# Kernel optimization log

Hardware: AMD Instinct MI355X
Metric: run time of the kernel (lower is better)

The kernel has to match this reference:

```python
import jax, jax.numpy as jnp
import numpy as np

B, N, IN_DIM, H, D = 4, 2048, 128, 4, 64
LEAKY_SLOPE = 0.2
BN_EPS = 1e-5


def setup_inputs() -> dict:
    key = jax.random.key(0)
    k_h, k_W, k_a, k_adj = jax.random.split(key, 4)
    h = jax.random.normal(k_h, (B, N, IN_DIM), dtype=jnp.float32)
    # Linear weight (no bias): stored as [in_dim, H*D] for x @ W
    W = jax.random.normal(k_W, (IN_DIM, H * D), dtype=jnp.float32) * (1.0 / np.sqrt(IN_DIM))
    # attention vector a: [H, 2D] (xavier-ish scale)
    a = jax.random.normal(k_a, (H, 2 * D), dtype=jnp.float32) * (1.0 / np.sqrt(2 * D))
    # BatchNorm affine params (training-mode batch stats used in reference)
    gamma = jnp.ones((H * D,), dtype=jnp.float32)
    beta = jnp.zeros((H * D,), dtype=jnp.float32)
    adj = jax.random.randint(k_adj, (N, N), 0, 2, dtype=jnp.int32)
    return {"h": h, "W": W, "a": a, "gamma": gamma, "beta": beta, "adj": adj}


def reference(h, W, a, gamma, beta, adj):
    Bs, Ns, _ = h.shape
    # Wh: [B, H, N, D]
    Wh = (h @ W).reshape(Bs, Ns, H, D).transpose(0, 2, 1, 3)
    # Algebraic decomposition of the concat-attention:
    # e[b,h,i,j] = leaky(Wh[b,h,i]. a[h,:D] + Wh[b,h,j]. a[h,D:])
    src = jnp.einsum("bhnd,hd->bhn", Wh, a[:, :D])  # query-node term
    dst = jnp.einsum("bhnd,hd->bhn", Wh, a[:, D:])  # key-node term
    e = src[:, :, :, None] + dst[:, :, None, :]      # [B,H,N,N]
    e = jnp.where(e >= 0, e, LEAKY_SLOPE * e)        # LeakyReLU
    mask = (adj == 0)[None, None, :, :]
    e = jnp.where(mask, -jnp.inf, e)
    alpha = jax.nn.softmax(e, axis=-1)
    alpha = jnp.nan_to_num(alpha, nan=0.0)
    # dropout is identity in eval mode (deterministic reference)
    h_new = jnp.einsum("bhij,bhjd->bhid", alpha, Wh)  # [B,H,N,D]
    h_new = h_new.transpose(0, 2, 1, 3).reshape(Bs, Ns, H * D)
    # BatchNorm1d (training mode: biased batch statistics over B*N rows)
    flat = h_new.reshape(Bs * Ns, H * D)
    mean = jnp.mean(flat, axis=0)
    var = jnp.mean(jnp.square(flat - mean), axis=0)
    flat = (flat - mean) * jax.lax.rsqrt(var + BN_EPS) * gamma + beta
    out = flat.reshape(Bs, Ns, H * D)
    return jax.nn.elu(out)
```

## Files before the change

### kernel.cpp

```cpp
#include <hip/hip_runtime.h>

#define B_ 4
#define N_ 2048
#define IND_ 128
#define H_ 4
#define D_ 64
#define HD_ 256
#define LEAKY 0.2f
#define BNEPS 1e-5f
#define LOG2E 1.44269504088896340736f

typedef float f32x4 __attribute__((ext_vector_type(4)));
typedef short s16x8 __attribute__((ext_vector_type(8)));
typedef unsigned int u32x4 __attribute__((ext_vector_type(4)));

static __device__ __forceinline__ unsigned short f2bf(float f) {
  unsigned u = __builtin_bit_cast(unsigned, f);
  u = (u + 0x7fffu + ((u >> 16) & 1u)) >> 16;
  return (unsigned short)u;
}

__global__ __launch_bounds__(256) void k_pack_adj(const int* __restrict__ adj,
                                                  unsigned* __restrict__ bits,
                                                  float* __restrict__ zbuf,
                                                  const float* __restrict__ W,
                                                  unsigned short* __restrict__ wt) {
  if (blockIdx.x == 0) {
    for (int i = threadIdx.x; i < 512; i += 256) zbuf[i] = 0.f;
  }
  if (blockIdx.x < 128) {
    int kb = blockIdx.x;
    wt[(size_t)threadIdx.x * 128 + kb] = f2bf(W[(size_t)kb * 256 + threadIdx.x]);
  }
  int idx = blockIdx.x * 256 + threadIdx.x;
  int val = adj[idx] != 0;
  unsigned long long m = __ballot(val);
  int lane = threadIdx.x & 63;
  if (lane == 0)       bits[idx >> 5] = (unsigned)m;
  else if (lane == 32) bits[idx >> 5] = (unsigned)(m >> 32);
}

__global__ __launch_bounds__(256) void k_gemm(const float* __restrict__ h,
                                              const unsigned short* __restrict__ wt,
                                              const float* __restrict__ a,
                                              unsigned short* __restrict__ wht,
                                              float* __restrict__ src,
                                              float* __restrict__ dst) {
  int t = threadIdx.x;
  int w = t >> 6, lane = t & 63, m = lane & 15, g = lane >> 4;
  int r0 = blockIdx.x * 16;
  int b = r0 >> 11, n0 = r0 & 2047;
  int hh = w;

  s16x8 Af[4][4];
  const s16x8* wtp = (const s16x8*)wt;
#pragma unroll
  for (int chf = 0; chf < 4; chf++) {
    int ch = w * 64 + chf * 16 + m;
#pragma unroll
    for (int ks = 0; ks < 4; ks++)
      Af[chf][ks] = wtp[(ch * 128 + ks * 32 + g * 8) >> 3];
  }
  s16x8 Bf[4];
#pragma unroll
  for (int ks = 0; ks < 4; ks++) {
    const float* hp = h + (size_t)(r0 + m) * 128 + ks * 32 + g * 8;
    f32x4 h0 = *(const f32x4*)hp;
    f32x4 h1 = *(const f32x4*)(hp + 4);
    u32x4 bu;
#pragma unroll
    for (int e = 0; e < 4; e++) {
      float lo = (e < 2) ? h0[2 * e] : h1[2 * e - 4];
      float hi = (e < 2) ? h0[2 * e + 1] : h1[2 * e - 3];
      unsigned rr_;
      asm("v_cvt_pk_bf16_f32 %0, %1, %2" : "=v"(rr_) : "v"(lo), "v"(hi));
      bu[e] = rr_;
    }
    Bf[ks] = __builtin_bit_cast(s16x8, bu);
  }

  f32x4 acc[4];
#pragma unroll
  for (int chf = 0; chf < 4; chf++) acc[chf] = (f32x4){0.f, 0.f, 0.f, 0.f};
#pragma unroll
  for (int ks = 0; ks < 4; ks++)
#pragma unroll
    for (int chf = 0; chf < 4; chf++)
      acc[chf] = __builtin_amdgcn_mfma_f32_16x16x32_bf16(Af[chf][ks], Bf[ks], acc[chf], 0, 0, 0);

  size_t obase = ((size_t)((b * 4 + hh) * 64)) * 2048 + n0 + m;
#pragma unroll
  for (int chf = 0; chf < 4; chf++) {
    int d = chf * 16 + g * 4;
#pragma unroll
    for (int reg = 0; reg < 4; reg++)
      wht[obase + (size_t)(d + reg) * 2048] = f2bf(acc[chf][reg]);
  }

  float sv = 0.f, dv = 0.f;
#pragma unroll
  for (int chf = 0; chf < 4; chf++)
#pragma unroll
    for (int reg = 0; reg < 4; reg++) {
      int d = chf * 16 + g * 4 + reg;
      float whv = acc[chf][reg];
      sv = fmaf(whv, a[hh * 128 + d] * LOG2E, sv);
      dv = fmaf(whv, a[hh * 128 + 64 + d] * LOG2E, dv);
    }
  sv += __shfl_xor(sv, 16); sv += __shfl_xor(sv, 32);
  dv += __shfl_xor(dv, 16); dv += __shfl_xor(dv, 32);
  if (g == 0) {
    src[(size_t)(b * 4 + hh) * 2048 + n0 + m] = sv;
    dst[(size_t)(b * 4 + hh) * 2048 + n0 + m] = dv;
  }
}

__global__ __launch_bounds__(256) void k_attn(const unsigned* __restrict__ adjb,
                                              const unsigned short* __restrict__ wht,
                                              const float* __restrict__ src,
                                              const float* __restrict__ dst,
                                              float* __restrict__ hnew,
                                              float* __restrict__ chsum,
                                              float* __restrict__ chsq) {
  __shared__ unsigned adj_lds[64 * 65];
  __shared__ u32x4 whb4[1024];
  __shared__ float ul[2048], vl[2048];
  __shared__ float redS[256], redQ[256];

  int t = threadIdx.x;
  int bid = blockIdx.x;
  int bh = bid & 15, it = bid >> 4;
  int b = bh >> 2, hh = bh & 3;
  int i0 = it * 64;
  int w = t >> 6, lane = t & 63, m = lane & 15, g = lane >> 4;

  for (int idx = t; idx < 64 * 64; idx += 256) {
    int r = idx >> 6, wd = idx & 63;
    adj_lds[r * 65 + wd] = adjb[(size_t)(i0 + r) * 64 + wd];
  }
  {
    const f32x4* dg = (const f32x4*)(dst + (size_t)bh * 2048);
    f32x4 d0 = dg[2 * t], d1 = dg[2 * t + 1];
    f32x4 u0, u1, v0, v1;
#pragma unroll
    for (int e = 0; e < 4; e++) {
      u0[e] = __builtin_amdgcn_exp2f(d0[e]);
      v0[e] = __builtin_amdgcn_exp2f(0.2f * d0[e]);
      u1[e] = __builtin_amdgcn_exp2f(d1[e]);
      v1[e] = __builtin_amdgcn_exp2f(0.2f * d1[e]);
    }
    ((f32x4*)ul)[2 * t] = u0;  ((f32x4*)ul)[2 * t + 1] = u1;
    ((f32x4*)vl)[2 * t] = v0;  ((f32x4*)vl)[2 * t + 1] = v1;
  }

  float srcL = src[(size_t)bh * 2048 + i0 + w * 16 + m];
  float Af = __builtin_amdgcn_exp2f(srcL);
  float Bf = __builtin_amdgcn_exp2f(LEAKY * srcL);

  s16x8 bones;
#pragma unroll
  for (int e = 0; e < 8; e++) bones[e] = (short)0x3F80;

  f32x4 acc[4], accd;
#pragma unroll
  for (int db = 0; db < 4; db++) acc[db] = (f32x4){0.f, 0.f, 0.f, 0.f};
  accd = (f32x4){0.f, 0.f, 0.f, 0.f};

  char* wbase = (char*)whb4;
  int r_ = t >> 2, ch_ = t & 3;
  const char* gbase = (const char*)(wht + (size_t)(bh * 64 + r_) * 2048);
  int sw = (r_ & 7) << 4;
  u32x4 R0, R1;

#define LOADT(jt_) { const u32x4* gp = (const u32x4*)(gbase + (size_t)(jt_) * 128 + ch_ * 32); \
                     R0 = gp[0]; R1 = gp[1]; }
#define WRITET(pb_) { char* wb_ = (pb_); \
                      *(u32x4*)(wb_ + r_ * 128 + ((ch_ * 32) ^ sw)) = R0; \
                      *(u32x4*)(wb_ + r_ * 128 + ((ch_ * 32 + 16) ^ sw)) = R1; }

  LOADT(0); WRITET(wbase); LOADT(1);

  for (int jt = 0; jt < 32; jt++) {
    int cur = jt & 1;
    __syncthreads();
    if (jt < 31) WRITET(wbase + (cur ^ 1) * 8192);
    if (jt < 30) LOADT(jt + 2);
    const char* wbufc = wbase + cur * 8192;

#pragma unroll
    for (int ks = 0; ks < 2; ks++) {
      unsigned adjw = adj_lds[(w * 16 + m) * 65 + jt * 2 + ks];
      unsigned bits = (adjw >> (g * 8)) & 0xffu;
      const float* up = &ul[jt * 64 + ks * 32 + g * 8];
      const float* vp = &vl[jt * 64 + ks * 32 + g * 8];
      f32x4 u0 = *(const f32x4*)up, u1 = *(const f32x4*)(up + 4);
      f32x4 v0 = *(const f32x4*)vp, v1 = *(const f32x4*)(vp + 4);
      float pm[8];
#pragma unroll
      for (int e = 0; e < 8; e++) {
        float ue = (e < 4) ? u0[e] : u1[e - 4];
        float ve = (e < 4) ? v0[e] : v1[e - 4];
        float p = fmaxf(Af * ue, Bf * ve);
        unsigned keep = (unsigned)(((int)(bits << (31 - e))) >> 31);
        pm[e] = __builtin_bit_cast(float, __builtin_bit_cast(unsigned, p) & keep);
      }
      u32x4 afu;
#pragma unroll
      for (int e2 = 0; e2 < 4; e2++) {
        unsigned rr_;
        asm("v_cvt_pk_bf16_f32 %0, %1, %2" : "=v"(rr_) : "v"(pm[2 * e2]), "v"(pm[2 * e2 + 1]));
        afu[e2] = rr_;
      }
      s16x8 af = __builtin_bit_cast(s16x8, afu);
#pragma unroll
      for (int db = 0; db < 4; db++) {
        int dl = db * 16 + m;
        int off = dl * 128 + ((ks * 64 + g * 16) ^ ((dl & 7) << 4));
        s16x8 bf = *(const s16x8*)(wbufc + off);
        acc[db] = __builtin_amdgcn_mfma_f32_16x16x32_bf16(af, bf, acc[db], 0, 0, 0);
      }
      accd = __builtin_amdgcn_mfma_f32_16x16x32_bf16(af, bones, accd, 0, 0, 0);
    }
  }
#undef LOADT
#undef WRITET

  float sums[4] = {0.f, 0.f, 0.f, 0.f}, sqs[4] = {0.f, 0.f, 0.f, 0.f};
#pragma unroll
  for (int r = 0; r < 4; r++) {
    float inv = accd[r] > 0.f ? 1.0f / accd[r] : 0.f;
    int n = i0 + w * 16 + 4 * g + r;
#pragma unroll
    for (int db = 0; db < 4; db++) {
      float val = acc[db][r] * inv;
      hnew[(size_t)(b * 2048 + n) * 256 + hh * 64 + db * 16 + m] = val;
      sums[db] += val;
      sqs[db] += val * val;
    }
  }
#pragma unroll
  for (int db = 0; db < 4; db++) {
    sums[db] += __shfl_xor(sums[db], 16); sums[db] += __shfl_xor(sums[db], 32);
    sqs[db]  += __shfl_xor(sqs[db], 16);  sqs[db]  += __shfl_xor(sqs[db], 32);
  }
  if (g == 0) {
#pragma unroll
    for (int db = 0; db < 4; db++) {
      redS[w * 64 + db * 16 + m] = sums[db];
      redQ[w * 64 + db * 16 + m] = sqs[db];
    }
  }
  __syncthreads();
  if (t < 64) {
    float ts2 = redS[t] + redS[64 + t] + redS[128 + t] + redS[192 + t];
    float tq = redQ[t] + redQ[64 + t] + redQ[128 + t] + redQ[192 + t];
    atomicAdd(&chsum[hh * 64 + t], ts2);
    atomicAdd(&chsq[hh * 64 + t], tq);
  }
}

__global__ __launch_bounds__(256) void k_bn_elu(const float* __restrict__ hnew,
                                                const float* __restrict__ chsum,
                                                const float* __restrict__ chsq,
                                                const float* __restrict__ gamma,
                                                const float* __restrict__ beta,
                                                float* __restrict__ out) {
  int idx4 = blockIdx.x * 256 + threadIdx.x;
  f32x4 x = ((const f32x4*)hnew)[idx4];
  int c0 = (idx4 * 4) & 255;
  f32x4 s = *(const f32x4*)(chsum + c0);
  f32x4 sq = *(const f32x4*)(chsq + c0);
  f32x4 gm = *(const f32x4*)(gamma + c0);
  f32x4 bt = *(const f32x4*)(beta + c0);
  f32x4 y;
#pragma unroll
  for (int e = 0; e < 4; e++) {
    float mean = s[e] * (1.0f / 8192.0f);
    float var = sq[e] * (1.0f / 8192.0f) - mean * mean;
    float sc = gm[e] * rsqrtf(var + BNEPS);
    float v = (x[e] - mean) * sc + bt[e];
    y[e] = v > 0.f ? v : expm1f(v);
  }
  ((f32x4*)out)[idx4] = y;
}

extern "C" void kernel_launch(void* const* d_in, const int* in_sizes, int n_in,
                              void* d_out, int out_size, void* d_ws, size_t ws_size,
                              hipStream_t stream) {
  const float* h = (const float*)d_in[0];
  const float* W = (const float*)d_in[1];
  const float* a = (const float*)d_in[2];
  const float* gamma = (const float*)d_in[3];
  const float* beta = (const float*)d_in[4];
  const int* adj = (const int*)d_in[5];

  char* ws = (char*)d_ws;
  unsigned* adjb = (unsigned*)ws;
  unsigned short* wht = (unsigned short*)(ws + (512 << 10));
  float* src = (float*)(ws + (512 << 10) + (4 << 20));
  float* dst = src + 16 * 2048;
  float* chsum = dst + 16 * 2048;
  float* chsq = chsum + 256;
  unsigned short* wt = (unsigned short*)(ws + (512 << 10) + (4 << 20) + (512 << 10));
  float* hnew = (float*)(ws + (512 << 10) + (5 << 20));

  k_pack_adj<<<(N_ * N_) / 256, 256, 0, stream>>>(adj, adjb, chsum, W, wt);
  k_gemm<<<(B_ * N_) / 16, 256, 0, stream>>>(h, wt, a, wht, src, dst);
  k_attn<<<B_ * H_ * (N_ / 64), 256, 0, stream>>>(adjb, wht, src, dst,
                                                  hnew, chsum, chsq);
  k_bn_elu<<<(B_ * N_ * HD_) / 1024, 256, 0, stream>>>(hnew, chsum, chsq,
                                                       gamma, beta, (float*)d_out);
}
```

Measured before the change: 57.86 us.

## Merge pre-kernels and restructure attention with async LDS ring and 32x32 MFMA

Fuses adjacency bit-packing and the projection GEMM into one launch, with the GEMM now converting W to bf16 in-kernel instead of through a separate transposed buffer. The attention kernel replaces register-staged double buffering with a 4-slot ring filled by global_load_lds direct-to-LDS loads, synchronised by explicit vmcnt waits. It also switches to 32x32x16 MFMA tiles with a split over j between wave pairs and a cross-wave LDS reduction, and streams adjacency words from global memory instead of staging them in LDS. These changes aim to cut launch overhead, LDS write traffic and barrier stalls, at the cost of an extra reduction step and hand-tuned wait counts that are easy to get wrong.

Result: no change. 57.65 us (-0.4%).

```diff
diff --git a/kernel.cpp b/kernel.cpp
--- a/kernel.cpp
+++ b/kernel.cpp
@@ -11,6 +11,7 @@
 #define LOG2E 1.44269504088896340736f
 
 typedef float f32x4 __attribute__((ext_vector_type(4)));
+typedef float f32x16 __attribute__((ext_vector_type(16)));
 typedef short s16x8 __attribute__((ext_vector_type(8)));
 typedef unsigned int u32x4 __attribute__((ext_vector_type(4)));
 
@@ -20,46 +21,52 @@
   return (unsigned short)u;
 }
 
-__global__ __launch_bounds__(256) void k_pack_adj(const int* __restrict__ adj,
-                                                  unsigned* __restrict__ bits,
-                                                  float* __restrict__ zbuf,
-                                                  const float* __restrict__ W,
-                                                  unsigned short* __restrict__ wt) {
-  if (blockIdx.x == 0) {
-    for (int i = threadIdx.x; i < 512; i += 256) zbuf[i] = 0.f;
-  }
-  if (blockIdx.x < 128) {
-    int kb = blockIdx.x;
-    wt[(size_t)threadIdx.x * 128 + kb] = f2bf(W[(size_t)kb * 256 + threadIdx.x]);
-  }
-  int idx = blockIdx.x * 256 + threadIdx.x;
-  int val = adj[idx] != 0;
-  unsigned long long m = __ballot(val);
-  int lane = threadIdx.x & 63;
-  if (lane == 0)       bits[idx >> 5] = (unsigned)m;
-  else if (lane == 32) bits[idx >> 5] = (unsigned)(m >> 32);
-}
-
-__global__ __launch_bounds__(256) void k_gemm(const float* __restrict__ h,
-                                              const unsigned short* __restrict__ wt,
-                                              const float* __restrict__ a,
-                                              unsigned short* __restrict__ wht,
-                                              float* __restrict__ src,
-                                              float* __restrict__ dst) {
+__global__ __launch_bounds__(256) void k_pre(const int* __restrict__ adj,
+                                             const float* __restrict__ W,
+                                             const float* __restrict__ h,
+                                             const float* __restrict__ a,
+                                             unsigned* __restrict__ bits,
+                                             float* __restrict__ zbuf,
+                                             unsigned short* __restrict__ wht,
+                                             float* __restrict__ src,
+                                             float* __restrict__ dst) {
   int t = threadIdx.x;
+  if (blockIdx.x >= 512) {
+    int pidx = blockIdx.x - 512;
+    if (pidx == 0) {
+      for (int i = t; i < 512; i += 256) zbuf[i] = 0.f;
+    }
+    int idx = pidx * 256 + t;
+    int val = adj[idx] != 0;
+    unsigned long long mm = __ballot(val);
+    int lane = t & 63;
+    if (lane == 0)       bits[idx >> 5] = (unsigned)mm;
+    else if (lane == 32) bits[idx >> 5] = (unsigned)(mm >> 32);
+    return;
+  }
   int w = t >> 6, lane = t & 63, m = lane & 15, g = lane >> 4;
   int r0 = blockIdx.x * 16;
   int b = r0 >> 11, n0 = r0 & 2047;
   int hh = w;
 
   s16x8 Af[4][4];
-  const s16x8* wtp = (const s16x8*)wt;
 #pragma unroll
   for (int chf = 0; chf < 4; chf++) {
-    int ch = w * 64 + chf * 16 + m;
-#pragma unroll
-    for (int ks = 0; ks < 4; ks++)
-      Af[chf][ks] = wtp[(ch * 128 + ks * 32 + g * 8) >> 3];
+    int chl = w * 64 + chf * 16 + m;
+#pragma unroll
+    for (int ks = 0; ks < 4; ks++) {
+      int k0 = ks * 32 + g * 8;
+      u32x4 au;
+#pragma unroll
+      for (int e2 = 0; e2 < 4; e2++) {
+        float lo = W[(size_t)(k0 + 2 * e2) * 256 + chl];
+        float hi = W[(size_t)(k0 + 2 * e2 + 1) * 256 + chl];
+        unsigned rr_;
+        asm("v_cvt_pk_bf16_f32 %0, %1, %2" : "=v"(rr_) : "v"(lo), "v"(hi));
+        au[e2] = rr_;
+      }
+      Af[chf][ks] = __builtin_bit_cast(s16x8, au);
+    }
   }
   s16x8 Bf[4];
 #pragma unroll
@@ -122,22 +129,19 @@
                                               float* __restrict__ hnew,
                                               float* __restrict__ chsum,
                                               float* __restrict__ chsq) {
-  __shared__ unsigned adj_lds[64 * 65];
-  __shared__ u32x4 whb4[1024];
+  __shared__ char ring[4 * 8192];
   __shared__ float ul[2048], vl[2048];
-  __shared__ float redS[256], redQ[256];
+  __shared__ float redS[128], redQ[128];
 
   int t = threadIdx.x;
   int bid = blockIdx.x;
   int bh = bid & 15, it = bid >> 4;
   int b = bh >> 2, hh = bh & 3;
   int i0 = it * 64;
-  int w = t >> 6, lane = t & 63, m = lane & 15, g = lane >> 4;
-
-  for (int idx = t; idx < 64 * 64; idx += 256) {
-    int r = idx >> 6, wd = idx & 63;
-    adj_lds[r * 65 + wd] = adjb[(size_t)(i0 + r) * 64 + wd];
-  }
+  int q = t >> 6, lane = t & 63;
+  int l31 = lane & 31, l5 = lane >> 5;
+  int iq = q >> 1, jq = q & 1;
+
   {
     const f32x4* dg = (const f32x4*)(dst + (size_t)bh * 2048);
     f32x4 d0 = dg[2 * t], d1 = dg[2 * t + 1];
@@ -153,55 +157,72 @@
     ((f32x4*)vl)[2 * t] = v0;  ((f32x4*)vl)[2 * t + 1] = v1;
   }
 
-  float srcL = src[(size_t)bh * 2048 + i0 + w * 16 + m];
-  float Af = __builtin_amdgcn_exp2f(srcL);
-  float Bf = __builtin_amdgcn_exp2f(LEAKY * srcL);
+  int row_i = i0 + iq * 32 + l31;
+  float srcL = src[(size_t)bh * 2048 + row_i];
+  float Afc = __builtin_amdgcn_exp2f(srcL);
+  float Bfc = __builtin_amdgcn_exp2f(LEAKY * srcL);
 
   s16x8 bones;
 #pragma unroll
   for (int e = 0; e < 8; e++) bones[e] = (short)0x3F80;
 
-  f32x4 acc[4], accd;
-#pragma unroll
-  for (int db = 0; db < 4; db++) acc[db] = (f32x4){0.f, 0.f, 0.f, 0.f};
-  accd = (f32x4){0.f, 0.f, 0.f, 0.f};
-
-  char* wbase = (char*)whb4;
-  int r_ = t >> 2, ch_ = t & 3;
-  const char* gbase = (const char*)(wht + (size_t)(bh * 64 + r_) * 2048);
-  int sw = (r_ & 7) << 4;
-  u32x4 R0, R1;
-
-#define LOADT(jt_) { const u32x4* gp = (const u32x4*)(gbase + (size_t)(jt_) * 128 + ch_ * 32); \
-                     R0 = gp[0]; R1 = gp[1]; }
-#define WRITET(pb_) { char* wb_ = (pb_); \
-                      *(u32x4*)(wb_ + r_ * 128 + ((ch_ * 32) ^ sw)) = R0; \
-                      *(u32x4*)(wb_ + r_ * 128 + ((ch_ * 32 + 16) ^ sw)) = R1; }
-
-  LOADT(0); WRITET(wbase); LOADT(1);
+  f32x16 acc0, acc1, accd;
+#pragma unroll
+  for (int i = 0; i < 16; i++) { acc0[i] = 0.f; acc1[i] = 0.f; accd[i] = 0.f; }
+
+  int rg = q * 16 + (lane >> 3);
+  int csw = ((lane & 7) ^ ((lane >> 3) & 7)) << 4;
+  const char* gsrc0 = (const char*)wht + (size_t)(bh * 64 + rg) * 4096 + csw;
+  const char* gsrc1 = gsrc0 + 8 * 4096;
+  char* ldst0 = ring + q * 2048;
+  char* ldst1 = ldst0 + 1024;
+
+#define GLD(gp_, lp_) __builtin_amdgcn_global_load_lds( \
+    (const __attribute__((address_space(1))) void*)(gp_), \
+    (__attribute__((address_space(3))) void*)(lp_), 16, 0, 0)
+#define GLOADT(jt_) do { int sl_ = (jt_) & 3; \
+    GLD(gsrc0 + (jt_) * 128, ldst0 + sl_ * 8192); \
+    GLD(gsrc1 + (jt_) * 128, ldst1 + sl_ * 8192); } while (0)
+
+  const unsigned* adjp = adjb + (size_t)row_i * 64 + jq;
+
+  int xsw = (l31 & 7) << 4;
+  int xc0 = (jq * 64 + l5 * 16) ^ xsw;
+  int xc1 = (jq * 64 + 32 + l5 * 16) ^ xsw;
+  int dbase0 = l31 * 128;
+  int dbase1 = (32 + l31) * 128;
+  int uvbase = jq * 32 + l5 * 8;
+
+  unsigned aw0 = adjp[0], aw1 = adjp[2], aw2 = adjp[4], awN = 0;
+  GLOADT(0); GLOADT(1); GLOADT(2);
+  __syncthreads();
 
   for (int jt = 0; jt < 32; jt++) {
-    int cur = jt & 1;
-    __syncthreads();
-    if (jt < 31) WRITET(wbase + (cur ^ 1) * 8192);
-    if (jt < 30) LOADT(jt + 2);
-    const char* wbufc = wbase + cur * 8192;
-
-#pragma unroll
-    for (int ks = 0; ks < 2; ks++) {
-      unsigned adjw = adj_lds[(w * 16 + m) * 65 + jt * 2 + ks];
-      unsigned bits = (adjw >> (g * 8)) & 0xffu;
-      const float* up = &ul[jt * 64 + ks * 32 + g * 8];
-      const float* vp = &vl[jt * 64 + ks * 32 + g * 8];
-      f32x4 u0 = *(const f32x4*)up, u1 = *(const f32x4*)(up + 4);
-      f32x4 v0 = *(const f32x4*)vp, v1 = *(const f32x4*)(vp + 4);
+    if (jt >= 1) {
+      if (jt <= 29)      asm volatile("s_waitcnt vmcnt(6)" ::: "memory");
+      else if (jt == 30) asm volatile("s_waitcnt vmcnt(3)" ::: "memory");
+      else               asm volatile("s_waitcnt vmcnt(0)" ::: "memory");
+      __builtin_amdgcn_s_barrier();
+    }
+    if (jt <= 28) { awN = adjp[2 * (jt + 3)]; GLOADT(jt + 3); }
+
+    const char* rb = ring + (jt & 3) * 8192;
+    const float* uj = ul + jt * 64 + uvbase;
+    const float* vj = vl + jt * 64 + uvbase;
+#pragma unroll
+    for (int c = 0; c < 2; c++) {
+      unsigned bitsv = (aw0 >> (c * 16 + l5 * 8)) & 0xffu;
+      f32x4 u0 = *(const f32x4*)(uj + c * 16);
+      f32x4 u1 = *(const f32x4*)(uj + c * 16 + 4);
+      f32x4 v0 = *(const f32x4*)(vj + c * 16);
+      f32x4 v1 = *(const f32x4*)(vj + c * 16 + 4);
       float pm[8];
 #pragma unroll
       for (int e = 0; e < 8; e++) {
         float ue = (e < 4) ? u0[e] : u1[e - 4];
         float ve = (e < 4) ? v0[e] : v1[e - 4];
-        float p = fmaxf(Af * ue, Bf * ve);
-        unsigned keep = (unsigned)(((int)(bits << (31 - e))) >> 31);
+        float p = fmaxf(Afc * ue, Bfc * ve);
+        unsigned keep = (unsigned)(((int)(bitsv << (31 - e))) >> 31);
         pm[e] = __builtin_bit_cast(float, __builtin_bit_cast(unsigned, p) & keep);
       }
       u32x4 afu;
@@ -212,48 +233,58 @@
         afu[e2] = rr_;
       }
       s16x8 af = __builtin_bit_cast(s16x8, afu);
-#pragma unroll
-      for (int db = 0; db < 4; db++) {
-        int dl = db * 16 + m;
-        int off = dl * 128 + ((ks * 64 + g * 16) ^ ((dl & 7) << 4));
-        s16x8 bf = *(const s16x8*)(wbufc + off);
-        acc[db] = __builtin_amdgcn_mfma_f32_16x16x32_bf16(af, bf, acc[db], 0, 0, 0);
-      }
-      accd = __builtin_amdgcn_mfma_f32_16x16x32_bf16(af, bones, accd, 0, 0, 0);
-    }
-  }
-#undef LOADT
-#undef WRITET
-
-  float sums[4] = {0.f, 0.f, 0.f, 0.f}, sqs[4] = {0.f, 0.f, 0.f, 0.f};
-#pragma unroll
-  for (int r = 0; r < 4; r++) {
-    float inv = accd[r] > 0.f ? 1.0f / accd[r] : 0.f;
-    int n = i0 + w * 16 + 4 * g + r;
-#pragma unroll
-    for (int db = 0; db < 4; db++) {
-      float val = acc[db][r] * inv;
-      hnew[(size_t)(b * 2048 + n) * 256 + hh * 64 + db * 16 + m] = val;
-      sums[db] += val;
-      sqs[db] += val * val;
-    }
-  }
-#pragma unroll
-  for (int db = 0; db < 4; db++) {
-    sums[db] += __shfl_xor(sums[db], 16); sums[db] += __shfl_xor(sums[db], 32);
-    sqs[db]  += __shfl_xor(sqs[db], 16);  sqs[db]  += __shfl_xor(sqs[db], 32);
-  }
-  if (g == 0) {
-#pragma unroll
-    for (int db = 0; db < 4; db++) {
-      redS[w * 64 + db * 16 + m] = sums[db];
-      redQ[w * 64 + db * 16 + m] = sqs[db];
+      int xc = c ? xc1 : xc0;
+      s16x8 bf0 = *(const s16x8*)(rb + dbase0 + xc);
+      s16x8 bf1 = *(const s16x8*)(rb + dbase1 + xc);
+      acc0 = __builtin_amdgcn_mfma_f32_32x32x16_bf16(af, bf0, acc0, 0, 0, 0);
+      acc1 = __builtin_amdgcn_mfma_f32_32x32x16_bf16(af, bf1, acc1, 0, 0, 0);
+      accd = __builtin_amdgcn_mfma_f32_32x32x16_bf16(af, bones, accd, 0, 0, 0);
+    }
+    aw0 = aw1; aw1 = aw2; aw2 = awN;
+  }
+#undef GLOADT
+#undef GLD
+
+  __syncthreads();
+  float* bi = (float*)ring + iq * (32 * 66);
+  if (jq == 1) {
+#pragma unroll
+    for (int reg = 0; reg < 16; reg++) {
+      int cr = (reg & 3) + 8 * (reg >> 2) + 4 * l5;
+      bi[cr * 66 + l31] = acc0[reg];
+      bi[cr * 66 + 32 + l31] = acc1[reg];
+      if (l31 == 0) bi[cr * 66 + 64] = accd[reg];
+    }
+  }
+  __syncthreads();
+  if (jq == 0) {
+    float sums0 = 0.f, sums1 = 0.f, sqs0 = 0.f, sqs1 = 0.f;
+#pragma unroll
+    for (int reg = 0; reg < 16; reg++) {
+      int cr = (reg & 3) + 8 * (reg >> 2) + 4 * l5;
+      float a0 = acc0[reg] + bi[cr * 66 + l31];
+      float a1 = acc1[reg] + bi[cr * 66 + 32 + l31];
+      float dtot = accd[reg] + bi[cr * 66 + 64];
+      float inv = dtot > 0.f ? 1.0f / dtot : 0.f;
+      float o0 = a0 * inv, o1 = a1 * inv;
+      int n = i0 + iq * 32 + cr;
+      float* hp = hnew + ((size_t)(b * 2048 + n)) * 256 + hh * 64;
+      hp[l31] = o0;
+      hp[32 + l31] = o1;
+      sums0 += o0; sums1 += o1;
+      sqs0 += o0 * o0; sqs1 += o1 * o1;
+    }
+    sums0 += __shfl_xor(sums0, 32); sums1 += __shfl_xor(sums1, 32);
+    sqs0 += __shfl_xor(sqs0, 32);   sqs1 += __shfl_xor(sqs1, 32);
+    if (lane < 32) {
+      redS[iq * 64 + l31] = sums0;  redS[iq * 64 + 32 + l31] = sums1;
+      redQ[iq * 64 + l31] = sqs0;   redQ[iq * 64 + 32 + l31] = sqs1;
     }
   }
   __syncthreads();
   if (t < 64) {
-    float ts2 = redS[t] + redS[64 + t] + redS[128 + t] + redS[192 + t];
-    float tq = redQ[t] + redQ[64 + t] + redQ[128 + t] + redQ[192 + t];
+    float ts2 = redS[t] + redS[64 + t];
+    float tq = redQ[t] + redQ[64 + t];
     atomicAdd(&chsum[hh * 64 + t], ts2);
     atomicAdd(&chsq[hh * 64 + t], tq);
   }
@@ -301,11 +332,10 @@
   float* dst = src + 16 * 2048;
   float* chsum = dst + 16 * 2048;
   float* chsq = chsum + 256;
-  unsigned short* wt = (unsigned short*)(ws + (512 << 10) + (4 << 20) + (512 << 10));
   float* hnew = (float*)(ws + (512 << 10) + (5 << 20));
 
-  k_pack_adj<<<(N_ * N_) / 256, 256, 0, stream>>>(adj, adjb, chsum, W, wt);
-  k_gemm<<<(B_ * N_) / 16, 256, 0, stream>>>(h, wt, a, wht, src, dst);
+  k_pre<<<512 + (N_ * N_) / 256, 256, 0, stream>>>(adj, W, h, a, adjb, chsum,
+                                                   wht, src, dst);
   k_attn<<<B_ * H_ * (N_ / 64), 256, 0, stream>>>(adjb, wht, src, dst,
                                                   hnew, chsum, chsq);
   k_bn_elu<<<(B_ * N_ * HD_) / 1024, 256, 0, stream>>>(hnew, chsum, chsq,
```
